# Optimization experiments

Measured on AMD Instinct MI355X. Metric: run time of the kernel, lower is better.

Reference implementation:

```python
import jax, jax.numpy as jnp
import numpy as np

N_NODES = 50000
EPS_BN = 1e-5


def _glorot(key, shape):
    fan_in, fan_out = shape[0], shape[1]
    lim = jnp.sqrt(6.0 / (fan_in + fan_out))
    return jax.random.uniform(key, shape, jnp.float32, -lim, lim)


def setup_inputs() -> dict:
    key = jax.random.key(0)
    ks = jax.random.split(key, 12)
    x = jax.random.normal(ks[0], (N_NODES, 128), jnp.float32)
    y = jax.random.normal(ks[1], (256, 1), jnp.float32)
    edge_index = jax.random.randint(ks[2], (2, 800000), 0, N_NODES, jnp.int64)
    return {
        "x": x,
        "y": y,
        "edge_index": edge_index,
        # GCNConv weights (in_dim, out_dim) + bias
        "W1": _glorot(ks[3], (128, 128)), "b1": jnp.zeros((128,), jnp.float32),
        "W2": _glorot(ks[4], (128, 128)), "b2": jnp.zeros((128,), jnp.float32),
        "W3": _glorot(ks[5], (128, 64)),  "b3": jnp.zeros((64,), jnp.float32),
        # target MLP: BatchNorm1d(1) -> Linear(1,128) -> ReLU -> Dropout -> Linear(128,64)
        "bn_gamma": jnp.ones((1,), jnp.float32), "bn_beta": jnp.zeros((1,), jnp.float32),
        "Wm1": _glorot(ks[6], (1, 128)),  "bm1": jnp.zeros((128,), jnp.float32),
        "Wm2": _glorot(ks[7], (128, 64)), "bm2": jnp.zeros((64,), jnp.float32),
    }


def gcn_conv(h, W, b, src, dst, deg_isqrt, n):
    # PyG GCNConv: x' = D^-1/2 (A+I) D^-1/2 (x W) + b, self-loops included in src/dst
    h = h @ W  # [n, out]
    norm = (deg_isqrt[src] * deg_isqrt[dst])[:, None]  # [E, 1]
    msg = h[src] * norm  # gather + scale, [E, out]
    out = jax.ops.segment_sum(msg, dst, num_segments=n)  # scatter-add
    return out + b


def reference(x, y, edge_index, W1, b1, W2, b2, W3, b3, bn_gamma, bn_beta, Wm1, bm1, Wm2, bm2):
    n = x.shape[0]
    loops = jnp.arange(n, dtype=edge_index.dtype)
    src = jnp.concatenate([edge_index[0], loops])
    dst = jnp.concatenate([edge_index[1], loops])
    deg = jax.ops.segment_sum(jnp.ones_like(dst, dtype=x.dtype), dst, num_segments=n)
    deg_isqrt = jnp.where(deg > 0, jax.lax.rsqrt(deg), 0.0)

    h = jax.nn.relu(gcn_conv(x, W1, b1, src, dst, deg_isqrt, n))
    h = jax.nn.relu(gcn_conv(h, W2, b2, src, dst, deg_isqrt, n))
    h = gcn_conv(h, W3, b3, src, dst, deg_isqrt, n)
    # transform_feat: normalize per-node embeddings (global_mean_pool result is discarded in source)
    x_emb = h / jnp.clip(jnp.linalg.norm(h, axis=1, keepdims=True), 1e-12)

    # target branch: BatchNorm1d (training-mode batch stats), Linear, ReLU, Dropout(eval=id), Linear
    mu = jnp.mean(y, axis=0, keepdims=True)
    var = jnp.var(y, axis=0, keepdims=True)
    yb = (y - mu) * jax.lax.rsqrt(var + EPS_BN) * bn_gamma + bn_beta
    t = jax.nn.relu(yb @ Wm1 + bm1)
    t = t @ Wm2 + bm2
    y_emb = t / jnp.clip(jnp.linalg.norm(t, axis=1, keepdims=True), 1e-12)
    return (x_emb, y_emb)
```

## Files before the change

### kernel.cpp

```cpp
#include <hip/hip_runtime.h>
#include <hip/hip_bf16.h>

typedef __attribute__((ext_vector_type(8))) short short8;
typedef __attribute__((ext_vector_type(4))) float f32x4;

__device__ __forceinline__ ushort f2bf(float f) {
    union { float f; uint u; } v; v.f = f;
    uint u = v.u;
    return (ushort)((u + 0x7fffu + ((u >> 16) & 1u)) >> 16);
}
__device__ __forceinline__ float bf_lo(uint u) { return __uint_as_float(u << 16); }
__device__ __forceinline__ float bf_hi(uint u) { return __uint_as_float(u & 0xffff0000u); }
__device__ __forceinline__ float lane_bcast_f(float v, int j) {
    return __uint_as_float(__builtin_amdgcn_readlane(__float_as_uint(v), j));
}

template <int COLS, bool F32IN>
__device__ __forceinline__ void gemm_body(const void* __restrict__ Xin,
                                          const ushort* __restrict__ Wt,
                                          ushort* __restrict__ Y, int n,
                                          int bid, char* smem) {
    constexpr int LDW = 136;
    ushort* sX = (ushort*)smem;
    ushort* sW = sX + 64 * LDW;
    const int tid = threadIdx.x;
    const int row0 = bid * 64;

    if (F32IN) {
        const float* Xf = (const float*)Xin;
#pragma unroll
        for (int i = 0; i < 8; ++i) {
            int idx = i * 256 + tid;
            int r = idx >> 5, kc = idx & 31;
            int gr = min(row0 + r, n - 1);
            float4 v = *(const float4*)&Xf[(size_t)gr * 128 + kc * 4];
            ushort4 o;
            o.x = f2bf(v.x); o.y = f2bf(v.y); o.z = f2bf(v.z); o.w = f2bf(v.w);
            *(ushort4*)&sX[r * LDW + kc * 4] = o;
        }
    } else {
        const ushort* Xb = (const ushort*)Xin;
#pragma unroll
        for (int i = 0; i < 4; ++i) {
            int idx = i * 256 + tid;
            int r = idx >> 4, kc = idx & 15;
            int gr = min(row0 + r, n - 1);
            uint4 v = *(const uint4*)&Xb[(size_t)gr * 128 + kc * 8];
            *(uint4*)&sX[r * LDW + kc * 8] = v;
        }
    }
#pragma unroll
    for (int c = tid; c < COLS * 16; c += 256) {
        int r = c >> 4, kc = c & 15;
        uint4 v = *(const uint4*)&Wt[(size_t)r * 128 + kc * 8];
        *(uint4*)&sW[r * LDW + kc * 8] = v;
    }
    __syncthreads();

    constexpr int NT = (COLS == 128) ? 2 : 1;
    constexpr int WN = COLS / 4;
    const int w = tid >> 6;
    const int lane = tid & 63;
    const int lm = lane & 15;
    const int kq = lane >> 4;

    f32x4 acc[4][NT];
#pragma unroll
    for (int mt = 0; mt < 4; ++mt)
#pragma unroll
        for (int ntn = 0; ntn < NT; ++ntn) acc[mt][ntn] = (f32x4){0.f, 0.f, 0.f, 0.f};

#pragma unroll
    for (int ks = 0; ks < 4; ++ks) {
        const int k0 = ks * 32 + kq * 8;
        short8 bfr[NT];
#pragma unroll
        for (int ntn = 0; ntn < NT; ++ntn)
            bfr[ntn] = *(const short8*)&sW[(w * WN + ntn * 16 + lm) * LDW + k0];
#pragma unroll
        for (int mt = 0; mt < 4; ++mt) {
            short8 afr = *(const short8*)&sX[(mt * 16 + lm) * LDW + k0];
#pragma unroll
            for (int ntn = 0; ntn < NT; ++ntn)
                acc[mt][ntn] = __builtin_amdgcn_mfma_f32_16x16x32_bf16(afr, bfr[ntn], acc[mt][ntn], 0, 0, 0);
        }
    }

#pragma unroll
    for (int mt = 0; mt < 4; ++mt) {
        int r_base = row0 + mt * 16 + kq * 4;
#pragma unroll
        for (int ntn = 0; ntn < NT; ++ntn) {
            int col = w * WN + ntn * 16 + lm;
#pragma unroll
            for (int rr = 0; rr < 4; ++rr) {
                int r = r_base + rr;
                if (r < n) Y[(size_t)r * COLS + col] = f2bf(acc[mt][ntn][rr]);
            }
        }
    }
}

#define PCHUNK 4096

__global__ __launch_bounds__(256) void k_partition(const int* __restrict__ src,
                                                   const int* __restrict__ dst, int E,
                                                   int nbuck, int cap, int pblocks,
                                                   int* __restrict__ gcur,
                                                   uint* __restrict__ part,
                                                   const float* __restrict__ W1,
                                                   const float* __restrict__ W2,
                                                   const float* __restrict__ W3,
                                                   ushort* __restrict__ wt1,
                                                   ushort* __restrict__ wt2,
                                                   ushort* __restrict__ wt3) {
    __shared__ int hist[256];
    __shared__ int base[256];
    __shared__ int cnt2[256];
    const int tid = threadIdx.x;

    if ((int)blockIdx.x >= pblocks) {
        int i = (blockIdx.x - pblocks) * 256 + tid;
        if (i < 16384) {
            int k = i >> 7, nn = i & 127;
            wt1[nn * 128 + k] = f2bf(W1[i]);
        } else if (i < 32768) {
            int j = i - 16384;
            int k = j >> 7, nn = j & 127;
            wt2[nn * 128 + k] = f2bf(W2[j]);
        } else if (i < 40960) {
            int j = i - 32768;
            int k = j >> 6, nn = j & 63;
            wt3[nn * 128 + k] = f2bf(W3[j]);
        }
        return;
    }

    const int s0 = blockIdx.x * PCHUNK;
    const int send = min(s0 + PCHUNK, E);
    hist[tid] = 0;
    cnt2[tid] = 0;
    __syncthreads();
    for (int i = s0 + tid; i < send; i += 256) {
        int d = dst[i];
        atomicAdd(&hist[d >> 8], 1);
    }
    __syncthreads();
    if (tid < nbuck && hist[tid] > 0) base[tid] = atomicAdd(&gcur[tid], hist[tid]);
    __syncthreads();
    for (int i = s0 + tid; i < send; i += 256) {
        int d = dst[i];
        int s = src[i];
        int k = d >> 8;
        int r = base[k] + atomicAdd(&cnt2[k], 1);
        if (r < cap) part[(size_t)k * cap + r] = ((uint)d << 16) | (uint)s;
    }
}

__global__ __launch_bounds__(256) void k_sort_gemm1(const uint* __restrict__ part,
                                                    const int* __restrict__ gcur,
                                                    int nbuck, int cap, int n,
                                                    int* __restrict__ rowptr,
                                                    float* __restrict__ dis,
                                                    int* __restrict__ csr,
                                                    const float* __restrict__ x,
                                                    const ushort* __restrict__ wt1,
                                                    ushort* __restrict__ bufA) {
    __shared__ char smem[(64 + 128) * 136 * 2];
    const int tid = threadIdx.x;

    if ((int)blockIdx.x >= nbuck) {
        gemm_body<128, true>(x, wt1, bufA, n, blockIdx.x - nbuck, smem);
        return;
    }

    int* hist  = (int*)smem;
    int* pfx   = hist + 256;
    int* sscan = pfx + 256;
    const int b = blockIdx.x;

    int gv = (tid < nbuck) ? min(gcur[tid], cap) : 0;
    sscan[tid] = gv;
    __syncthreads();
    for (int off = 1; off < 256; off <<= 1) {
        int t = (tid >= off) ? sscan[tid - off] : 0;
        __syncthreads();
        sscan[tid] += t;
        __syncthreads();
    }
    const int outbase = (b == 0) ? 0 : sscan[b - 1];
    const int sz = min(gcur[b], cap);
    const uint* seg = part + (size_t)b * cap;

    hist[tid] = 0;
    __syncthreads();
    for (int i = tid; i < sz; i += 256) atomicAdd(&hist[(seg[i] >> 16) & 255], 1);
    __syncthreads();

    int cnt_t = hist[tid];
    pfx[tid] = cnt_t;
    __syncthreads();
    for (int off = 1; off < 256; off <<= 1) {
        int t = (tid >= off) ? pfx[tid - off] : 0;
        __syncthreads();
        pfx[tid] += t;
        __syncthreads();
    }
    int excl = pfx[tid] - cnt_t;

    int node = b * 256 + tid;
    if (node < n) {
        rowptr[node] = outbase + excl;
        dis[node] = rsqrtf((float)(cnt_t + 1));
        if (node == n - 1) rowptr[n] = outbase + excl + cnt_t;
    }
    __syncthreads();
    pfx[tid] = excl;
    hist[tid] = 0;
    __syncthreads();
    for (int i = tid; i < sz; i += 256) {
        uint p = seg[i];
        int j = (p >> 16) & 255;
        int r = atomicAdd(&hist[j], 1);
        csr[outbase + pfx[j] + r] = (int)(p & 0xffffu);
    }
}

template <int COLS, bool F32IN>
__global__ __launch_bounds__(256) void gemm_mfma(const void* __restrict__ Xin,
                                                 const ushort* __restrict__ Wt,
                                                 ushort* __restrict__ Y, int n) {
    __shared__ char smem[(64 + COLS) * 136 * 2];
    gemm_body<COLS, F32IN>(Xin, Wt, Y, n, blockIdx.x, smem);
}

template <bool RELU>
__global__ __launch_bounds__(256) void agg128(const ushort* __restrict__ H,
                                              const float* __restrict__ dis,
                                              const int* __restrict__ rowptr,
                                              const int* __restrict__ csr,
                                              const float* __restrict__ bias,
                                              uint* __restrict__ out, int n) {
    const int wid = blockIdx.x * 4 + (threadIdx.x >> 6);
    const int lane = threadIdx.x & 63;
    if (wid >= n) return;
    const int v = wid;
    const float dv = dis[v];
    const int e0 = rowptr[v];
    const int e1 = rowptr[v + 1];

    const uint* Hu = (const uint*)H;
    uint h0 = Hu[(size_t)v * 64 + lane];
    float ax = dv * bf_lo(h0), ay = dv * bf_hi(h0);

    int e = e0;
    while (e < e1) {
        const int c = min(e1 - e, 64);
        int sidx = 0; float sw = 0.0f;
        if (lane < c) { sidx = csr[e + lane]; sw = dis[sidx]; }
        int j = 0;
        for (; j + 16 <= c; j += 16) {
            uint hv[16]; float w[16];
#pragma unroll
            for (int u = 0; u < 16; ++u) {
                int s = __builtin_amdgcn_readlane(sidx, j + u);
                w[u] = lane_bcast_f(sw, j + u);
                hv[u] = Hu[(size_t)s * 64 + lane];
            }
#pragma unroll
            for (int u = 0; u < 16; ++u) { ax += w[u] * bf_lo(hv[u]); ay += w[u] * bf_hi(hv[u]); }
        }
        for (; j + 4 <= c; j += 4) {
            uint hv[4]; float w[4];
#pragma unroll
            for (int u = 0; u < 4; ++u) {
                int s = __builtin_amdgcn_readlane(sidx, j + u);
                w[u] = lane_bcast_f(sw, j + u);
                hv[u] = Hu[(size_t)s * 64 + lane];
            }
#pragma unroll
            for (int u = 0; u < 4; ++u) { ax += w[u] * bf_lo(hv[u]); ay += w[u] * bf_hi(hv[u]); }
        }
        for (; j < c; ++j) {
            int s = __builtin_amdgcn_readlane(sidx, j);
            float w = lane_bcast_f(sw, j);
            uint hh = Hu[(size_t)s * 64 + lane];
            ax += w * bf_lo(hh); ay += w * bf_hi(hh);
        }
        e += c;
    }

    float2 b = ((const float2*)bias)[lane];
    float rx = dv * ax + b.x;
    float ry = dv * ay + b.y;
    if (RELU) { rx = fmaxf(rx, 0.f); ry = fmaxf(ry, 0.f); }
    uint packed = (uint)f2bf(rx) | ((uint)f2bf(ry) << 16);
    out[(size_t)v * 64 + lane] = packed;
}

__global__ __launch_bounds__(256) void agg64_final(const ushort* __restrict__ H,
                                                   const float* __restrict__ dis,
                                                   const int* __restrict__ rowptr,
                                                   const int* __restrict__ csr,
                                                   const float* __restrict__ bias,
                                                   float* __restrict__ out, int n, int agrid,
                                                   const float* __restrict__ y,
                                                   const float* __restrict__ gamma,
                                                   const float* __restrict__ beta,
                                                   const float* __restrict__ Wm1,
                                                   const float* __restrict__ bm1,
                                                   const float* __restrict__ Wm2,
                                                   const float* __restrict__ bm2,
                                                   float* __restrict__ out_y) {
    __shared__ float red[256];
    __shared__ float t1[128];
    __shared__ float s_mu, s_var;
    const int tid = threadIdx.x;

    if ((int)blockIdx.x >= agrid) {
        float yv = y[tid];
        red[tid] = yv;
        __syncthreads();
        for (int s = 128; s > 0; s >>= 1) {
            if (tid < s) red[tid] += red[tid + s];
            __syncthreads();
        }
        if (tid == 0) s_mu = red[0] * (1.0f / 256.0f);
        __syncthreads();
        float mu = s_mu;
        float d = yv - mu;
        red[tid] = d * d;
        __syncthreads();
        for (int s = 128; s > 0; s >>= 1) {
            if (tid < s) red[tid] += red[tid + s];
            __syncthreads();
        }
        if (tid == 0) s_var = red[0] * (1.0f / 256.0f);
        __syncthreads();

        const int row = blockIdx.x - agrid;
        float yb = (y[row] - mu) * rsqrtf(s_var + 1e-5f) * gamma[0] + beta[0];
        if (tid < 128) t1[tid] = fmaxf(yb * Wm1[tid] + bm1[tid], 0.0f);
        __syncthreads();
        if (tid < 64) {
            float acc = bm2[tid];
#pragma unroll 8
            for (int c = 0; c < 128; ++c) acc += t1[c] * Wm2[c * 64 + tid];
            float ss = acc * acc;
#pragma unroll
            for (int m = 1; m < 64; m <<= 1) ss += __shfl_xor(ss, m, 64);
            out_y[row * 64 + tid] = acc / fmaxf(sqrtf(ss), 1e-12f);
        }
        return;
    }

    const int wid = blockIdx.x * 4 + (tid >> 6);
    const int lane = tid & 63;
    if (wid >= n) return;
    const int v = wid;
    const float dv = dis[v];
    const int e0 = rowptr[v];
    const int e1 = rowptr[v + 1];

    float acc = dv * bf_lo((uint)H[(size_t)v * 64 + lane]);

    int e = e0;
    while (e < e1) {
        const int c = min(e1 - e, 64);
        int sidx = 0; float sw = 0.0f;
        if (lane < c) { sidx = csr[e + lane]; sw = dis[sidx]; }
        int j = 0;
        for (; j + 16 <= c; j += 16) {
            ushort hv[16]; float w[16];
#pragma unroll
            for (int u = 0; u < 16; ++u) {
                int s = __builtin_amdgcn_readlane(sidx, j + u);
                w[u] = lane_bcast_f(sw, j + u);
                hv[u] = H[(size_t)s * 64 + lane];
            }
#pragma unroll
            for (int u = 0; u < 16; ++u) acc += w[u] * bf_lo((uint)hv[u]);
        }
        for (; j < c; ++j) {
            int s = __builtin_amdgcn_readlane(sidx, j);
            float w = lane_bcast_f(sw, j);
            acc += w * bf_lo((uint)H[(size_t)s * 64 + lane]);
        }
        e += c;
    }

    float r = dv * acc + bias[lane];
    float ss = r * r;
#pragma unroll
    for (int m = 1; m < 64; m <<= 1) ss += __shfl_xor(ss, m, 64);
    r = r / fmaxf(sqrtf(ss), 1e-12f);
    out[(size_t)v * 64 + lane] = r;
}

extern "C" void kernel_launch(void* const* d_in, const int* in_sizes, int n_in,
                              void* d_out, int out_size, void* d_ws, size_t ws_size,
                              hipStream_t stream) {
    const float* x     = (const float*)d_in[0];
    const float* y     = (const float*)d_in[1];
    const int*   edge  = (const int*)d_in[2];
    const float* W1    = (const float*)d_in[3];
    const float* b1    = (const float*)d_in[4];
    const float* W2    = (const float*)d_in[5];
    const float* b2    = (const float*)d_in[6];
    const float* W3    = (const float*)d_in[7];
    const float* b3    = (const float*)d_in[8];
    const float* bng   = (const float*)d_in[9];
    const float* bnb   = (const float*)d_in[10];
    const float* Wm1   = (const float*)d_in[11];
    const float* bm1   = (const float*)d_in[12];
    const float* Wm2   = (const float*)d_in[13];
    const float* bm2   = (const float*)d_in[14];

    const int n = in_sizes[0] / 128;
    const int E = in_sizes[2] / 2;
    const int* src = edge;
    const int* dst = edge + E;

    const int nbuck = (n + 255) / 256;
    const int cap = E / nbuck + E / nbuck / 4 + 1024;

    size_t off = 0;
    auto carve = [&](size_t bytes) {
        size_t p = off;
        off = (off + bytes + 255) & ~(size_t)255;
        return p;
    };
    char* ws = (char*)d_ws;
    int*    gcur    = (int*)(ws + carve(256 * 4));
    uint*   part    = (uint*)(ws + carve((size_t)nbuck * cap * 4));
    int*    rowptr  = (int*)(ws + carve((size_t)(n + 1) * 4));
    int*    csr     = (int*)(ws + carve((size_t)E * 4));
    float*  dis     = (float*)(ws + carve((size_t)n * 4));
    ushort* wt1     = (ushort*)(ws + carve(128 * 128 * 2));
    ushort* wt2     = (ushort*)(ws + carve(128 * 128 * 2));
    ushort* wt3     = (ushort*)(ws + carve(64 * 128 * 2));
    ushort* bufA    = (ushort*)(ws + carve((size_t)n * 128 * 2));
    ushort* bufB    = (ushort*)(ws + carve((size_t)n * 128 * 2));
    ushort* bufC    = (ushort*)(ws + carve((size_t)n * 64 * 2));
    (void)ws_size; (void)n_in; (void)out_size;

    float* x_emb = (float*)d_out;
    float* y_emb = (float*)d_out + (size_t)n * 64;

    const int pblocks = (E + PCHUNK - 1) / PCHUNK;
    const int ggrid = (n + 63) / 64;
    const int agrid = (n + 3) / 4;

    hipMemsetAsync(gcur, 0, 256 * 4, stream);
    k_partition<<<pblocks + 160, 256, 0, stream>>>(src, dst, E, nbuck, cap, pblocks,
                                                   gcur, part, W1, W2, W3, wt1, wt2, wt3);
    k_sort_gemm1<<<nbuck + ggrid, 256, 0, stream>>>(part, gcur, nbuck, cap, n,
                                                    rowptr, dis, csr, x, wt1, bufA);

    agg128<true><<<agrid, 256, 0, stream>>>(bufA, dis, rowptr, csr, b1, (uint*)bufB, n);
    gemm_mfma<128, false><<<ggrid, 256, 0, stream>>>(bufB, wt2, bufA, n);
    agg128<true><<<agrid, 256, 0, stream>>>(bufA, dis, rowptr, csr, b2, (uint*)bufB, n);
    gemm_mfma<64, false><<<ggrid, 256, 0, stream>>>(bufB, wt3, bufC, n);
    agg64_final<<<agrid + 256, 256, 0, stream>>>(bufC, dis, rowptr, csr, b3, x_emb, n, agrid,
                                                 y, bng, bnb, Wm1, bm1, Wm2, bm2, y_emb);
}
```

Baseline: 248.6 us.

## Fuse GCN aggregation with following MFMA GEMM via shared-memory tile

Merges the layer-1/2 aggregation kernels with the next layer's weight GEMM. Each block of 4 waves aggregates 64 rows into LDS, then runs a bf16 MFMA against W2 or W3 and writes the projected result. This removes two launches and the global round trip of the intermediate activations. In exchange, parallelism drops: 782 blocks each doing 16 serial rows per wave, compared with 12500 blocks before. The W fragments are also read from global memory rather than LDS.

```diff
diff --git a/kernel.cpp b/kernel.cpp
--- a/kernel.cpp
+++ b/kernel.cpp
@@ -226,76 +226,115 @@
     }
 }
 
-template <int COLS, bool F32IN>
-__global__ __launch_bounds__(256) void gemm_mfma(const void* __restrict__ Xin,
-                                                 const ushort* __restrict__ Wt,
-                                                 ushort* __restrict__ Y, int n) {
-    __shared__ char smem[(64 + COLS) * 136 * 2];
-    gemm_body<COLS, F32IN>(Xin, Wt, Y, n, blockIdx.x, smem);
-}
-
-template <bool RELU>
-__global__ __launch_bounds__(256) void agg128(const ushort* __restrict__ H,
-                                              const float* __restrict__ dis,
-                                              const int* __restrict__ rowptr,
-                                              const int* __restrict__ csr,
-                                              const float* __restrict__ bias,
-                                              uint* __restrict__ out, int n) {
-    const int wid = blockIdx.x * 4 + (threadIdx.x >> 6);
-    const int lane = threadIdx.x & 63;
-    if (wid >= n) return;
-    const int v = wid;
-    const float dv = dis[v];
-    const int e0 = rowptr[v];
-    const int e1 = rowptr[v + 1];
-
+template <int COLS>
+__global__ __launch_bounds__(256) void agg_gemm(const ushort* __restrict__ H,
+                                                const float* __restrict__ dis,
+                                                const int* __restrict__ rowptr,
+                                                const int* __restrict__ csr,
+                                                const float* __restrict__ bias,
+                                                const ushort* __restrict__ Wt,
+                                                ushort* __restrict__ Y, int n) {
+    __shared__ ushort sX[64 * 136];
+    const int tid = threadIdx.x;
+    const int wv = tid >> 6;
+    const int lane = tid & 63;
+    const int row0 = blockIdx.x * 64;
     const uint* Hu = (const uint*)H;
-    uint h0 = Hu[(size_t)v * 64 + lane];
-    float ax = dv * bf_lo(h0), ay = dv * bf_hi(h0);
-
-    int e = e0;
-    while (e < e1) {
-        const int c = min(e1 - e, 64);
-        int sidx = 0; float sw = 0.0f;
-        if (lane < c) { sidx = csr[e + lane]; sw = dis[sidx]; }
-        int j = 0;
-        for (; j + 16 <= c; j += 16) {
-            uint hv[16]; float w[16];
-#pragma unroll
-            for (int u = 0; u < 16; ++u) {
-                int s = __builtin_amdgcn_readlane(sidx, j + u);
-                w[u] = lane_bcast_f(sw, j + u);
-                hv[u] = Hu[(size_t)s * 64 + lane];
+    const float2 bv = ((const float2*)bias)[lane];
+
+#pragma unroll 1
+    for (int i = 0; i < 16; ++i) {
+        const int lr = wv * 16 + i;
+        const int v = min(row0 + lr, n - 1);
+        const float dv = dis[v];
+        const int e0 = rowptr[v];
+        const int e1 = rowptr[v + 1];
+        uint h0 = Hu[(size_t)v * 64 + lane];
+        float ax = dv * bf_lo(h0), ay = dv * bf_hi(h0);
+
+        int e = e0;
+        while (e < e1) {
+            const int c = min(e1 - e, 64);
+            int sidx = 0; float sw = 0.0f;
+            if (lane < c) { sidx = csr[e + lane]; sw = dis[sidx]; }
+            int j = 0;
+            for (; j + 16 <= c; j += 16) {
+                uint hv[16]; float wgt[16];
+#pragma unroll
+                for (int u = 0; u < 16; ++u) {
+                    int s = __builtin_amdgcn_readlane(sidx, j + u);
+                    wgt[u] = lane_bcast_f(sw, j + u);
+                    hv[u] = Hu[(size_t)s * 64 + lane];
+                }
+#pragma unroll
+                for (int u = 0; u < 16; ++u) { ax += wgt[u] * bf_lo(hv[u]); ay += wgt[u] * bf_hi(hv[u]); }
             }
-#pragma unroll
-            for (int u = 0; u < 16; ++u) { ax += w[u] * bf_lo(hv[u]); ay += w[u] * bf_hi(hv[u]); }
-        }
-        for (; j + 4 <= c; j += 4) {
-            uint hv[4]; float w[4];
-#pragma unroll
-            for (int u = 0; u < 4; ++u) {
-                int s = __builtin_amdgcn_readlane(sidx, j + u);
-                w[u] = lane_bcast_f(sw, j + u);
-                hv[u] = Hu[(size_t)s * 64 + lane];
+            for (; j + 4 <= c; j += 4) {
+                uint hv[4]; float wgt[4];
+#pragma unroll
+                for (int u = 0; u < 4; ++u) {
+                    int s = __builtin_amdgcn_readlane(sidx, j + u);
+                    wgt[u] = lane_bcast_f(sw, j + u);
+                    hv[u] = Hu[(size_t)s * 64 + lane];
+                }
+#pragma unroll
+                for (int u = 0; u < 4; ++u) { ax += wgt[u] * bf_lo(hv[u]); ay += wgt[u] * bf_hi(hv[u]); }
             }
-#pragma unroll
-            for (int u = 0; u < 4; ++u) { ax += w[u] * bf_lo(hv[u]); ay += w[u] * bf_hi(hv[u]); }
-        }
-        for (; j < c; ++j) {
-            int s = __builtin_amdgcn_readlane(sidx, j);
-            float w = lane_bcast_f(sw, j);
-            uint hh = Hu[(size_t)s * 64 + lane];
-            ax += w * bf_lo(hh); ay += w * bf_hi(hh);
-        }
-        e += c;
-    }
-
-    float2 b = ((const float2*)bias)[lane];
-    float rx = dv * ax + b.x;
-    float ry = dv * ay + b.y;
-    if (RELU) { rx = fmaxf(rx, 0.f); ry = fmaxf(ry, 0.f); }
-    uint packed = (uint)f2bf(rx) | ((uint)f2bf(ry) << 16);
-    out[(size_t)v * 64 + lane] = packed;
+            for (; j < c; ++j) {
+                int s = __builtin_amdgcn_readlane(sidx, j);
+                float wg = lane_bcast_f(sw, j);
+                uint hh = Hu[(size_t)s * 64 + lane];
+                ax += wg * bf_lo(hh); ay += wg * bf_hi(hh);
+            }
+            e += c;
+        }
+
+        float rx = fmaxf(dv * ax + bv.x, 0.f);
+        float ry = fmaxf(dv * ay + bv.y, 0.f);
+        ((uint*)sX)[lr * 68 + lane] = (uint)f2bf(rx) | ((uint)f2bf(ry) << 16);
+    }
+    __syncthreads();
+
+    constexpr int NT = (COLS == 128) ? 2 : 1;
+    constexpr int WN = COLS / 4;
+    const int lm = lane & 15;
+    const int kq = lane >> 4;
+
+    f32x4 acc[4][NT];
+#pragma unroll
+    for (int mt = 0; mt < 4; ++mt)
+#pragma unroll
+        for (int ntn = 0; ntn < NT; ++ntn) acc[mt][ntn] = (f32x4){0.f, 0.f, 0.f, 0.f};
+
+#pragma unroll
+    for (int ks = 0; ks < 4; ++ks) {
+        const int k0 = ks * 32 + kq * 8;
+        short8 bfr[NT];
+#pragma unroll
+        for (int ntn = 0; ntn < NT; ++ntn)
+            bfr[ntn] = *(const short8*)&Wt[(size_t)(wv * WN + ntn * 16 + lm) * 128 + k0];
+#pragma unroll
+        for (int mt = 0; mt < 4; ++mt) {
+            short8 afr = *(const short8*)&sX[(mt * 16 + lm) * 136 + k0];
+#pragma unroll
+            for (int ntn = 0; ntn < NT; ++ntn)
+                acc[mt][ntn] = __builtin_amdgcn_mfma_f32_16x16x32_bf16(afr, bfr[ntn], acc[mt][ntn], 0, 0, 0);
+        }
+    }
+
+#pragma unroll
+    for (int mt = 0; mt < 4; ++mt) {
+        int r_base = row0 + mt * 16 + kq * 4;
+#pragma unroll
+        for (int ntn = 0; ntn < NT; ++ntn) {
+            int col = wv * WN + ntn * 16 + lm;
+#pragma unroll
+            for (int rr = 0; rr < 4; ++rr) {
+                int r = r_base + rr;
+                if (r < n) Y[(size_t)r * COLS + col] = f2bf(acc[mt][ntn][rr]);
+            }
+        }
+    }
 }
 
 __global__ __launch_bounds__(256) void agg64_final(const ushort* __restrict__ H,
@@ -457,10 +496,8 @@
     k_sort_gemm1<<<nbuck + ggrid, 256, 0, stream>>>(part, gcur, nbuck, cap, n,
                                                     rowptr, dis, csr, x, wt1, bufA);
 
-    agg128<true><<<agrid, 256, 0, stream>>>(bufA, dis, rowptr, csr, b1, (uint*)bufB, n);
-    gemm_mfma<128, false><<<ggrid, 256, 0, stream>>>(bufB, wt2, bufA, n);
-    agg128<true><<<agrid, 256, 0, stream>>>(bufA, dis, rowptr, csr, b2, (uint*)bufB, n);
-    gemm_mfma<64, false><<<ggrid, 256, 0, stream>>>(bufB, wt3, bufC, n);
+    agg_gemm<128><<<ggrid, 256, 0, stream>>>(bufA, dis, rowptr, csr, b1, wt2, bufB, n);
+    agg_gemm<64><<<ggrid, 256, 0, stream>>>(bufB, dis, rowptr, csr, b2, wt3, bufC, n);
     agg64_final<<<agrid + 256, 256, 0, stream>>>(bufC, dis, rowptr, csr, b3, x_emb, n, agrid,
                                                  y, bng, bnb, Wm1, bm1, Wm2, bm2, y_emb);
 }
```

Result: slower. 267.9 us (+7.7%).

## Prescale GEMM outputs by source degree and gather 16-byte rows per lane group

Applied to the files above, without the earlier changes.

The GEMMs for layers 2 and 3 now multiply each output row by its inverse-sqrt degree, so the following aggregations no longer load a per-edge dis[src] weight. Both aggregation kernels are restructured so that groups of lanes fetch whole neighbour rows with 16-byte loads, handling several edges at once, then combine the partial sums with cross-lane shuffles. The partition chunk size is also reduced to launch more partition blocks. This reorganises the memory access pattern of the gather, but adds shuffle reductions and pushes the extra scaling into bf16-rounded intermediates.

```diff
diff --git a/kernel.cpp b/kernel.cpp
--- a/kernel.cpp
+++ b/kernel.cpp
@@ -11,15 +11,13 @@
 }
 __device__ __forceinline__ float bf_lo(uint u) { return __uint_as_float(u << 16); }
 __device__ __forceinline__ float bf_hi(uint u) { return __uint_as_float(u & 0xffff0000u); }
-__device__ __forceinline__ float lane_bcast_f(float v, int j) {
-    return __uint_as_float(__builtin_amdgcn_readlane(__float_as_uint(v), j));
-}
-
-template <int COLS, bool F32IN>
+
+template <int COLS, bool F32IN, bool DISSCALE>
 __device__ __forceinline__ void gemm_body(const void* __restrict__ Xin,
                                           const ushort* __restrict__ Wt,
                                           ushort* __restrict__ Y, int n,
-                                          int bid, char* smem) {
+                                          int bid, char* smem,
+                                          const float* __restrict__ dis) {
     constexpr int LDW = 136;
     ushort* sX = (ushort*)smem;
     ushort* sW = sX + 64 * LDW;
@@ -90,18 +88,30 @@
     for (int mt = 0; mt < 4; ++mt) {
         int r_base = row0 + mt * 16 + kq * 4;
 #pragma unroll
-        for (int ntn = 0; ntn < NT; ++ntn) {
-            int col = w * WN + ntn * 16 + lm;
-#pragma unroll
-            for (int rr = 0; rr < 4; ++rr) {
-                int r = r_base + rr;
-                if (r < n) Y[(size_t)r * COLS + col] = f2bf(acc[mt][ntn][rr]);
+        for (int rr = 0; rr < 4; ++rr) {
+            int r = r_base + rr;
+            if (r < n) {
+                float dr = DISSCALE ? dis[r] : 1.0f;
+#pragma unroll
+                for (int ntn = 0; ntn < NT; ++ntn) {
+                    int col = w * WN + ntn * 16 + lm;
+                    Y[(size_t)r * COLS + col] = f2bf(acc[mt][ntn][rr] * dr);
+                }
             }
         }
     }
 }
 
-#define PCHUNK 4096
+template <int COLS, bool F32IN, bool DISSCALE>
+__global__ __launch_bounds__(256) void gemm_mfma(const void* __restrict__ Xin,
+                                                 const ushort* __restrict__ Wt,
+                                                 ushort* __restrict__ Y, int n,
+                                                 const float* __restrict__ dis) {
+    __shared__ char smem[(64 + COLS) * 136 * 2];
+    gemm_body<COLS, F32IN, DISSCALE>(Xin, Wt, Y, n, blockIdx.x, smem, dis);
+}
+
+#define PCHUNK 1024
 
 __global__ __launch_bounds__(256) void k_partition(const int* __restrict__ src,
                                                    const int* __restrict__ dst, int E,
@@ -170,7 +180,7 @@
     const int tid = threadIdx.x;
 
     if ((int)blockIdx.x >= nbuck) {
-        gemm_body<128, true>(x, wt1, bufA, n, blockIdx.x - nbuck, smem);
+        gemm_body<128, true, false>(x, wt1, bufA, n, blockIdx.x - nbuck, smem, nullptr);
         return;
     }
 
@@ -226,76 +236,85 @@
     }
 }
 
-template <int COLS, bool F32IN>
-__global__ __launch_bounds__(256) void gemm_mfma(const void* __restrict__ Xin,
-                                                 const ushort* __restrict__ Wt,
-                                                 ushort* __restrict__ Y, int n) {
-    __shared__ char smem[(64 + COLS) * 136 * 2];
-    gemm_body<COLS, F32IN>(Xin, Wt, Y, n, blockIdx.x, smem);
-}
-
-template <bool RELU>
+template <bool WITHDIS>
 __global__ __launch_bounds__(256) void agg128(const ushort* __restrict__ H,
                                               const float* __restrict__ dis,
                                               const int* __restrict__ rowptr,
                                               const int* __restrict__ csr,
                                               const float* __restrict__ bias,
-                                              uint* __restrict__ out, int n) {
+                                              ushort* __restrict__ Y, int n) {
     const int wid = blockIdx.x * 4 + (threadIdx.x >> 6);
+    if (wid >= n) return;
     const int lane = threadIdx.x & 63;
-    if (wid >= n) return;
+    const int g = lane >> 4;
+    const int q = lane & 15;
     const int v = wid;
+
+    const uint4* Hq = (const uint4*)H;
+    uint4 selfv = Hq[(size_t)v * 16 + q];
     const float dv = dis[v];
     const int e0 = rowptr[v];
     const int e1 = rowptr[v + 1];
 
-    const uint* Hu = (const uint*)H;
-    uint h0 = Hu[(size_t)v * 64 + lane];
-    float ax = dv * bf_lo(h0), ay = dv * bf_hi(h0);
+    float acc[8];
+#pragma unroll
+    for (int t = 0; t < 8; ++t) acc[t] = 0.f;
 
     int e = e0;
     while (e < e1) {
         const int c = min(e1 - e, 64);
         int sidx = 0; float sw = 0.0f;
-        if (lane < c) { sidx = csr[e + lane]; sw = dis[sidx]; }
-        int j = 0;
-        for (; j + 16 <= c; j += 16) {
-            uint hv[16]; float w[16];
-#pragma unroll
-            for (int u = 0; u < 16; ++u) {
-                int s = __builtin_amdgcn_readlane(sidx, j + u);
-                w[u] = lane_bcast_f(sw, j + u);
-                hv[u] = Hu[(size_t)s * 64 + lane];
+        if (lane < c) { sidx = csr[e + lane]; if (WITHDIS) sw = dis[sidx]; }
+#pragma unroll 1
+        for (int j = 0; j < c; j += 16) {
+            uint4 hv[4]; float wrow[4];
+#pragma unroll
+            for (int k = 0; k < 4; ++k) {
+                int srcLane = j + k * 4 + g;
+                int srow = __builtin_amdgcn_ds_bpermute(srcLane << 2, sidx);
+                if (WITHDIS)
+                    wrow[k] = __uint_as_float(__builtin_amdgcn_ds_bpermute(
+                        srcLane << 2, __float_as_uint(sw)));
+                else
+                    wrow[k] = (srcLane < c) ? 1.0f : 0.0f;
+                hv[k] = Hq[(size_t)srow * 16 + q];
             }
 #pragma unroll
-            for (int u = 0; u < 16; ++u) { ax += w[u] * bf_lo(hv[u]); ay += w[u] * bf_hi(hv[u]); }
-        }
-        for (; j + 4 <= c; j += 4) {
-            uint hv[4]; float w[4];
-#pragma unroll
-            for (int u = 0; u < 4; ++u) {
-                int s = __builtin_amdgcn_readlane(sidx, j + u);
-                w[u] = lane_bcast_f(sw, j + u);
-                hv[u] = Hu[(size_t)s * 64 + lane];
+            for (int k = 0; k < 4; ++k) {
+                acc[0] += wrow[k] * bf_lo(hv[k].x); acc[1] += wrow[k] * bf_hi(hv[k].x);
+                acc[2] += wrow[k] * bf_lo(hv[k].y); acc[3] += wrow[k] * bf_hi(hv[k].y);
+                acc[4] += wrow[k] * bf_lo(hv[k].z); acc[5] += wrow[k] * bf_hi(hv[k].z);
+                acc[6] += wrow[k] * bf_lo(hv[k].w); acc[7] += wrow[k] * bf_hi(hv[k].w);
             }
-#pragma unroll
-            for (int u = 0; u < 4; ++u) { ax += w[u] * bf_lo(hv[u]); ay += w[u] * bf_hi(hv[u]); }
-        }
-        for (; j < c; ++j) {
-            int s = __builtin_amdgcn_readlane(sidx, j);
-            float w = lane_bcast_f(sw, j);
-            uint hh = Hu[(size_t)s * 64 + lane];
-            ax += w * bf_lo(hh); ay += w * bf_hi(hh);
         }
         e += c;
     }
 
-    float2 b = ((const float2*)bias)[lane];
-    float rx = dv * ax + b.x;
-    float ry = dv * ay + b.y;
-    if (RELU) { rx = fmaxf(rx, 0.f); ry = fmaxf(ry, 0.f); }
-    uint packed = (uint)f2bf(rx) | ((uint)f2bf(ry) << 16);
-    out[(size_t)v * 64 + lane] = packed;
+#pragma unroll
+    for (int t = 0; t < 8; ++t) {
+        acc[t] += __shfl_xor(acc[t], 16);
+        acc[t] += __shfl_xor(acc[t], 32);
+    }
+    const float selfw = WITHDIS ? dv : 1.0f;
+    acc[0] += selfw * bf_lo(selfv.x); acc[1] += selfw * bf_hi(selfv.x);
+    acc[2] += selfw * bf_lo(selfv.y); acc[3] += selfw * bf_hi(selfv.y);
+    acc[4] += selfw * bf_lo(selfv.z); acc[5] += selfw * bf_hi(selfv.z);
+    acc[6] += selfw * bf_lo(selfv.w); acc[7] += selfw * bf_hi(selfv.w);
+
+    if (g == 0) {
+        float4 b0 = *(const float4*)&bias[q * 8];
+        float4 b1 = *(const float4*)&bias[q * 8 + 4];
+        float r0 = fmaxf(dv * acc[0] + b0.x, 0.f), r1 = fmaxf(dv * acc[1] + b0.y, 0.f);
+        float r2 = fmaxf(dv * acc[2] + b0.z, 0.f), r3 = fmaxf(dv * acc[3] + b0.w, 0.f);
+        float r4 = fmaxf(dv * acc[4] + b1.x, 0.f), r5 = fmaxf(dv * acc[5] + b1.y, 0.f);
+        float r6 = fmaxf(dv * acc[6] + b1.z, 0.f), r7 = fmaxf(dv * acc[7] + b1.w, 0.f);
+        uint4 o;
+        o.x = (uint)f2bf(r0) | ((uint)f2bf(r1) << 16);
+        o.y = (uint)f2bf(r2) | ((uint)f2bf(r3) << 16);
+        o.z = (uint)f2bf(r4) | ((uint)f2bf(r5) << 16);
+        o.w = (uint)f2bf(r6) | ((uint)f2bf(r7) << 16);
+        *(uint4*)&Y[(size_t)v * 128 + q * 8] = o;
+    }
 }
 
 __global__ __launch_bounds__(256) void agg64_final(const ushort* __restrict__ H,
@@ -355,46 +374,79 @@
     }
 
     const int wid = blockIdx.x * 4 + (tid >> 6);
+    if (wid >= n) return;
     const int lane = tid & 63;
-    if (wid >= n) return;
+    const int g = lane >> 3;
+    const int q = lane & 7;
     const int v = wid;
+
+    const uint4* Hq = (const uint4*)H;
+    uint4 selfv = Hq[(size_t)v * 8 + q];
     const float dv = dis[v];
     const int e0 = rowptr[v];
     const int e1 = rowptr[v + 1];
 
-    float acc = dv * bf_lo((uint)H[(size_t)v * 64 + lane]);
+    float acc[8];
+#pragma unroll
+    for (int t = 0; t < 8; ++t) acc[t] = 0.f;
 
     int e = e0;
     while (e < e1) {
         const int c = min(e1 - e, 64);
-        int sidx = 0; float sw = 0.0f;
-        if (lane < c) { sidx = csr[e + lane]; sw = dis[sidx]; }
-        int j = 0;
-        for (; j + 16 <= c; j += 16) {
-            ushort hv[16]; float w[16];
-#pragma unroll
-            for (int u = 0; u < 16; ++u) {
-                int s = __builtin_amdgcn_readlane(sidx, j + u);
-                w[u] = lane_bcast_f(sw, j + u);
-                hv[u] = H[(size_t)s * 64 + lane];
+        int sidx = 0;
+        if (lane < c) sidx = csr[e + lane];
+#pragma unroll 1
+        for (int j = 0; j < c; j += 16) {
+            uint4 hv[2]; float wrow[2];
+#pragma unroll
+            for (int k = 0; k < 2; ++k) {
+                int srcLane = j + k * 8 + g;
+                int srow = __builtin_amdgcn_ds_bpermute(srcLane << 2, sidx);
+                wrow[k] = (srcLane < c) ? 1.0f : 0.0f;
+                hv[k] = Hq[(size_t)srow * 8 + q];
             }
 #pragma unroll
-            for (int u = 0; u < 16; ++u) acc += w[u] * bf_lo((uint)hv[u]);
-        }
-        for (; j < c; ++j) {
-            int s = __builtin_amdgcn_readlane(sidx, j);
-            float w = lane_bcast_f(sw, j);
-            acc += w * bf_lo((uint)H[(size_t)s * 64 + lane]);
+            for (int k = 0; k < 2; ++k) {
+                acc[0] += wrow[k] * bf_lo(hv[k].x); acc[1] += wrow[k] * bf_hi(hv[k].x);
+                acc[2] += wrow[k] * bf_lo(hv[k].y); acc[3] += wrow[k] * bf_hi(hv[k].y);
+                acc[4] += wrow[k] * bf_lo(hv[k].z); acc[5] += wrow[k] * bf_hi(hv[k].z);
+                acc[6] += wrow[k] * bf_lo(hv[k].w); acc[7] += wrow[k] * bf_hi(hv[k].w);
+            }
         }
         e += c;
     }
 
-    float r = dv * acc + bias[lane];
-    float ss = r * r;
-#pragma unroll
-    for (int m = 1; m < 64; m <<= 1) ss += __shfl_xor(ss, m, 64);
-    r = r / fmaxf(sqrtf(ss), 1e-12f);
-    out[(size_t)v * 64 + lane] = r;
+#pragma unroll
+    for (int t = 0; t < 8; ++t) {
+        acc[t] += __shfl_xor(acc[t], 8);
+        acc[t] += __shfl_xor(acc[t], 16);
+        acc[t] += __shfl_xor(acc[t], 32);
+    }
+    acc[0] += bf_lo(selfv.x); acc[1] += bf_hi(selfv.x);
+    acc[2] += bf_lo(selfv.y); acc[3] += bf_hi(selfv.y);
+    acc[4] += bf_lo(selfv.z); acc[5] += bf_hi(selfv.z);
+    acc[6] += bf_lo(selfv.w); acc[7] += bf_hi(selfv.w);
+
+    float4 b0 = *(const float4*)&bias[q * 8];
+    float4 b1 = *(const float4*)&bias[q * 8 + 4];
+    float r[8];
+    r[0] = dv * acc[0] + b0.x; r[1] = dv * acc[1] + b0.y;
+    r[2] = dv * acc[2] + b0.z; r[3] = dv * acc[3] + b0.w;
+    r[4] = dv * acc[4] + b1.x; r[5] = dv * acc[5] + b1.y;
+    r[6] = dv * acc[6] + b1.z; r[7] = dv * acc[7] + b1.w;
+    float ss = 0.f;
+#pragma unroll
+    for (int t = 0; t < 8; ++t) ss += r[t] * r[t];
+    ss += __shfl_xor(ss, 1);
+    ss += __shfl_xor(ss, 2);
+    ss += __shfl_xor(ss, 4);
+    float inv = 1.0f / fmaxf(sqrtf(ss), 1e-12f);
+    if (g == 0) {
+        float4 o0 = {r[0] * inv, r[1] * inv, r[2] * inv, r[3] * inv};
+        float4 o1 = {r[4] * inv, r[5] * inv, r[6] * inv, r[7] * inv};
+        *(float4*)&out[(size_t)v * 64 + q * 8] = o0;
+        *(float4*)&out[(size_t)v * 64 + q * 8 + 4] = o1;
+    }
 }
 
 extern "C" void kernel_launch(void* const* d_in, const int* in_sizes, int n_in,
@@ -457,10 +509,10 @@
     k_sort_gemm1<<<nbuck + ggrid, 256, 0, stream>>>(part, gcur, nbuck, cap, n,
                                                     rowptr, dis, csr, x, wt1, bufA);
 
-    agg128<true><<<agrid, 256, 0, stream>>>(bufA, dis, rowptr, csr, b1, (uint*)bufB, n);
-    gemm_mfma<128, false><<<ggrid, 256, 0, stream>>>(bufB, wt2, bufA, n);
-    agg128<true><<<agrid, 256, 0, stream>>>(bufA, dis, rowptr, csr, b2, (uint*)bufB, n);
-    gemm_mfma<64, false><<<ggrid, 256, 0, stream>>>(bufB, wt3, bufC, n);
+    agg128<true><<<agrid, 256, 0, stream>>>(bufA, dis, rowptr, csr, b1, bufB, n);
+    gemm_mfma<128, false, true><<<ggrid, 256, 0, stream>>>(bufB, wt2, bufA, n, dis);
+    agg128<false><<<agrid, 256, 0, stream>>>(bufA, dis, rowptr, csr, b2, bufB, n);
+    gemm_mfma<64, false, true><<<ggrid, 256, 0, stream>>>(bufB, wt3, bufC, n, dis);
     agg64_final<<<agrid + 256, 256, 0, stream>>>(bufC, dis, rowptr, csr, b3, x_emb, n, agrid,
                                                  y, bng, bnb, Wm1, bm1, Wm2, bm2, y_emb);
 }
```

New measurement: 246.8 us. About the same (-0.7%).
